# Performance work log

Hardware: AMD Instinct MI355X
Metric: run time of the kernel (lower is better)

## Reference

```python
import jax, jax.numpy as jnp
import numpy as np

D = 128        # d_model (LayerNorm(128) hardcoded)
N_HEADS = 4
DIM_K = D // N_HEADS           # 32
HD = DIM_K // N_HEADS          # 8 = per-group dim after reshape(-1, B, S, HD)
NORM_FACT = 1.0 / np.sqrt(DIM_K)
HIDDEN = 512
LN_EPS = 1e-5
NEG_INF = -1e30


def layer_norm(x, g, b):
    mu = jnp.mean(x, axis=-1, keepdims=True)
    var = jnp.mean((x - mu) ** 2, axis=-1, keepdims=True)
    return (x - mu) * jax.lax.rsqrt(var + LN_EPS) * g + b


def lower_median(x):
    # torch.median(dim=-1) returns the LOWER of the two middle values for even n
    n = x.shape[-1]
    return jnp.sort(x, axis=-1)[..., (n - 1) // 2][..., None]


def cross_cov_attention(x, y, Wq, bq, Wk, bk, Wv, bv, Wo, bo):
    # x: query-side input [B,S,D]; y: key/value-side input [B,S,D]
    B, S, _ = x.shape
    Q = (x @ Wq + bq).reshape(-1, B, S, HD)   # [16,B,S,8] (raw row-major reshape, as in torch)
    K = (y @ Wk + bk).reshape(-1, B, S, HD)
    V = (y @ Wv + bv).reshape(-1, B, S, HD)
    Qn = Q / jnp.maximum(jnp.linalg.norm(Q, axis=-1, keepdims=True), 1e-12)
    Kn = K / jnp.maximum(jnp.linalg.norm(K, axis=-1, keepdims=True), 1e-12)
    # channel-wise cross-covariance: Q^T K over tokens -> [16,B,8,8]
    scores = jnp.einsum('gbsd,gbse->gbde', Qn, Kn) * NORM_FACT
    # median-threshold mask: keep entries strictly above the (lower) median of each row
    med = lower_median(scores)
    scores = jnp.where(scores - med > 0, scores, NEG_INF)
    probs = jax.nn.softmax(scores, axis=-1)
    # probs @ V^T -> [16,B,8,S]
    ao = jnp.einsum('gbde,gbse->gbds', probs, V)
    # torch: .transpose(-2,-1).transpose(1,2).view(B,S,-1)  == axes (g,b,d,s)->(g,s,b,d)->reshape
    ao = ao.transpose(0, 3, 1, 2).reshape(B, S, -1)  # [B,S,128]
    return ao @ Wo + bo


def setup_inputs() -> dict:
    key = jax.random.key(0)
    ks = jax.random.split(key, 16)
    B, S = 32, 4096
    s = 1.0 / np.sqrt(D)
    inp = {
        'q': jax.random.normal(ks[0], (B, S, D), jnp.float32),
        'v': jax.random.normal(ks[1], (B, S, D), jnp.float32),
        'Wq': jax.random.normal(ks[2], (D, D), jnp.float32) * s,
        'bq': jnp.zeros((D,), jnp.float32),
        'Wk': jax.random.normal(ks[3], (D, D), jnp.float32) * s,
        'bk': jnp.zeros((D,), jnp.float32),
        'Wv': jax.random.normal(ks[4], (D, D), jnp.float32) * s,
        'bv': jnp.zeros((D,), jnp.float32),
        'Wo': jax.random.normal(ks[5], (D, D), jnp.float32) * s,
        'bo': jnp.zeros((D,), jnp.float32),
        'ln_g': jnp.ones((D,), jnp.float32),
        'ln_b': jnp.zeros((D,), jnp.float32),
        'W1': jax.random.normal(ks[6], (D, HIDDEN), jnp.float32) * s,
        'b1': jnp.zeros((HIDDEN,), jnp.float32),
        'W2': jax.random.normal(ks[7], (HIDDEN, D), jnp.float32) * (1.0 / np.sqrt(HIDDEN)),
        'b2': jnp.zeros((D,), jnp.float32),
    }
    return inp


def reference(q, v, Wq, bq, Wk, bk, Wv, bv, Wo, bo, ln_g, ln_b, W1, b1, W2, b2):
    # Decoder.forward: add_norm(v, attn, y=q) -> add_norm(ffn) -> + v
    attn = cross_cov_attention(v, q, Wq, bq, Wk, bk, Wv, bv, Wo, bo)
    h = layer_norm(v + attn, ln_g, ln_b)          # dropout = identity (eval)
    ffn = jax.nn.gelu(h @ W1 + b1, approximate=False) @ W2 + b2
    h2 = layer_norm(h + ffn, ln_g, ln_b)          # same Add_Norm (shared LayerNorm params)
    return h2 + v
```

## Files before the change

### kernel.cpp

```cpp
#include <hip/hip_runtime.h>
#include <math.h>


typedef __bf16 bf16x8 __attribute__((ext_vector_type(8)));
typedef float f32x4 __attribute__((ext_vector_type(4)));
typedef unsigned short u16x8 __attribute__((ext_vector_type(8)));
typedef unsigned int u32x2 __attribute__((ext_vector_type(2)));
typedef unsigned int u32x4 __attribute__((ext_vector_type(4)));
typedef unsigned short ushort_t;

static constexpr int  DM   = 128;
static constexpr long NTOK = 131072;
static constexpr float NORMF = 0.17677669529663687f;

__device__ __forceinline__ unsigned short f2b(float x) {
    __bf16 b = (__bf16)x;
    return __builtin_bit_cast(unsigned short, b);
}
__device__ __forceinline__ float b2f(unsigned short h) {
    return __builtin_bit_cast(float, ((unsigned)h) << 16);
}
__device__ __forceinline__ float b2f_lo(unsigned u) {
    return __builtin_bit_cast(float, u << 16);
}
__device__ __forceinline__ float b2f_hi(unsigned u) {
    return __builtin_bit_cast(float, u & 0xffff0000u);
}
__device__ __forceinline__ unsigned pack2(float a, float b) {
    return (unsigned)f2b(a) | ((unsigned)f2b(b) << 16);
}
__device__ __forceinline__ f32x4 mfma16(bf16x8 a, bf16x8 b, f32x4 c) {
    return __builtin_amdgcn_mfma_f32_16x16x32_bf16(a, b, c, 0, 0, 0);
}
__device__ __forceinline__ int xb_off(int tok, int chunk) {
    int c = (chunk & 8) | ((chunk ^ tok) & 7);
    return tok * 128 + c * 8;
}
__device__ __forceinline__ float gelu_f(float x) {
    float x2 = x * x;
    float y = -x * fmaf(0.0713548162f, x2, 1.5957691216f);
    float e = __expf(y);
    return x * __builtin_amdgcn_rcpf(1.0f + e);
}

__global__ __launch_bounds__(256)
void k_wcvt(const float* __restrict__ W1, const float* __restrict__ W2,
            const float* __restrict__ Wo, const float* __restrict__ Wq,
            const float* __restrict__ Wk, const float* __restrict__ Wv,
            ushort_t* __restrict__ W1t, ushort_t* __restrict__ W2t,
            ushort_t* __restrict__ Wot,
            ushort_t* __restrict__ Wqh, ushort_t* __restrict__ Wql,
            ushort_t* __restrict__ Wkh, ushort_t* __restrict__ Wkl,
            ushort_t* __restrict__ Wvh, ushort_t* __restrict__ Wvl)
{
    int frag = blockIdx.x * 4 + (threadIdx.x >> 6);
    int l = threadIdx.x & 63;
    int lr = l & 15, lg = l >> 4;
    u16x8 v;
    if (frag < 128) {
        int ht = frag >> 2, ks = frag & 3;
        #pragma unroll
        for (int j = 0; j < 8; ++j)
            v[j] = f2b(W1[(ks * 32 + lg * 8 + j) * 512 + ht * 16 + lr]);
        *(u16x8*)(W1t + ((long)frag * 64 + l) * 8) = v;
    } else if (frag < 256) {
        int f = frag - 128;
        int ot = f >> 4, ks = f & 15;
        #pragma unroll
        for (int j = 0; j < 8; ++j)
            v[j] = f2b(W2[(ks * 32 + lg * 8 + j) * 128 + ot * 16 + lr]);
        *(u16x8*)(W2t + ((long)f * 64 + l) * 8) = v;
    } else if (frag < 288) {
        int f = frag - 256;
        int ot = f >> 2, ks = f & 3;
        #pragma unroll
        for (int j = 0; j < 8; ++j)
            v[j] = f2b(Wo[(ks * 32 + lg * 8 + j) * 128 + ot * 16 + lr]);
        *(u16x8*)(Wot + ((long)f * 64 + l) * 8) = v;
    } else {
        int f = frag - 288;
        const float* S = (f < 32) ? Wq : (f < 64) ? Wk : Wv;
        ushort_t* dh = (f < 32) ? Wqh : (f < 64) ? Wkh : Wvh;
        ushort_t* dl = (f < 32) ? Wql : (f < 64) ? Wkl : Wvl;
        int fl = f & 31, ot = fl >> 2, ks = fl & 3;
        u16x8 vh, vl;
        #pragma unroll
        for (int j = 0; j < 8; ++j) {
            float x = S[(ks * 32 + lg * 8 + j) * 128 + ot * 16 + lr];
            __bf16 bh = (__bf16)x;
            vh[j] = __builtin_bit_cast(unsigned short, bh);
            vl[j] = f2b(x - (float)bh);
        }
        *(u16x8*)(dh + ((long)fl * 64 + l) * 8) = vh;
        *(u16x8*)(dl + ((long)fl * 64 + l) * 8) = vl;
    }
}

__global__ __launch_bounds__(256, 2)
void k_qkvs(const float* __restrict__ qin, const float* __restrict__ vin,
            const ushort_t* __restrict__ Wqh, const ushort_t* __restrict__ Wql,
            const ushort_t* __restrict__ Wkh, const ushort_t* __restrict__ Wkl,
            const ushort_t* __restrict__ Wvh, const ushort_t* __restrict__ Wvl,
            const float* __restrict__ bq, const float* __restrict__ bk,
            const float* __restrict__ bv,
            ushort_t* __restrict__ Vbf, float* __restrict__ scoreacc)
{
    __shared__ __align__(16) char smem[65536];
    ushort_t* vhi = (ushort_t*)smem;
    ushort_t* vlo = vhi + 8192;
    ushort_t* qhi = vlo + 8192;
    ushort_t* qlo = qhi + 8192;
    ushort_t* Vt  = (ushort_t*)smem;
    float*    red = (float*)(smem + 16384);

    const int tid = threadIdx.x;
    const int w = tid >> 6, l = tid & 63;
    const int lr = l & 15, lg = l >> 4;
    const long tok0 = (long)blockIdx.x * 64;

    #pragma unroll
    for (int i = 0; i < 4; ++i) {
        int e = tid + i * 256;
        int tok = e >> 4, c = e & 15;
        long base = (tok0 + tok) * DM + c * 8;
        int xo = xb_off(tok, c);
        {
            float4 a0 = *(const float4*)(vin + base);
            float4 a1 = *(const float4*)(vin + base + 4);
            float xs[8] = {a0.x, a0.y, a0.z, a0.w, a1.x, a1.y, a1.z, a1.w};
            u16x8 hi, lo;
            #pragma unroll
            for (int jj = 0; jj < 8; ++jj) {
                __bf16 bh = (__bf16)xs[jj];
                hi[jj] = __builtin_bit_cast(unsigned short, bh);
                lo[jj] = f2b(xs[jj] - (float)bh);
            }
            *(u16x8*)(vhi + xo) = hi;
            *(u16x8*)(vlo + xo) = lo;
        }
        {
            float4 a0 = *(const float4*)(qin + base);
            float4 a1 = *(const float4*)(qin + base + 4);
            float xs[8] = {a0.x, a0.y, a0.z, a0.w, a1.x, a1.y, a1.z, a1.w};
            u16x8 hi, lo;
            #pragma unroll
            for (int jj = 0; jj < 8; ++jj) {
                __bf16 bh = (__bf16)xs[jj];
                hi[jj] = __builtin_bit_cast(unsigned short, bh);
                lo[jj] = f2b(xs[jj] - (float)bh);
            }
            *(u16x8*)(qhi + xo) = hi;
            *(u16x8*)(qlo + xo) = lo;
        }
    }
    __syncthreads();

    float qv[2][4][4];
    {
        f32x4 acc[2][4];
        #pragma unroll
        for (int ot = 0; ot < 2; ++ot)
            #pragma unroll
            for (int tt = 0; tt < 4; ++tt) acc[ot][tt] = (f32x4){0,0,0,0};
        #pragma unroll
        for (int ks = 0; ks < 4; ++ks) {
            bf16x8 wh[2], wl[2];
            #pragma unroll
            for (int ot = 0; ot < 2; ++ot) {
                int fi = (((w * 2 + ot) * 4 + ks) * 64 + l) * 8;
                wh[ot] = *(const bf16x8*)(Wqh + fi);
                wl[ot] = *(const bf16x8*)(Wql + fi);
            }
            #pragma unroll
            for (int tt = 0; tt < 4; ++tt) {
                int xo = xb_off(tt * 16 + lr, ks * 4 + lg);
                bf16x8 xh = *(const bf16x8*)(vhi + xo);
                bf16x8 xl = *(const bf16x8*)(vlo + xo);
                #pragma unroll
                for (int ot = 0; ot < 2; ++ot) {
                    acc[ot][tt] = mfma16(wh[ot], xh, acc[ot][tt]);
                    acc[ot][tt] = mfma16(wh[ot], xl, acc[ot][tt]);
                    acc[ot][tt] = mfma16(wl[ot], xh, acc[ot][tt]);
                }
            }
        }
        #pragma unroll
        for (int ot = 0; ot < 2; ++ot) {
            f32x4 bqv = *(const f32x4*)(bq + w * 32 + ot * 16 + lg * 4);
            #pragma unroll
            for (int tt = 0; tt < 4; ++tt) {
                float s2 = 0.f;
                #pragma unroll
                for (int r = 0; r < 4; ++r) {
                    float x = acc[ot][tt][r] + bqv[r];
                    qv[ot][tt][r] = x;
                    s2 = fmaf(x, x, s2);
                }
                s2 += __shfl_xor(s2, 16);
                float inv = 1.0f / fmaxf(sqrtf(s2), 1e-12f);
                #pragma unroll
                for (int r = 0; r < 4; ++r) qv[ot][tt][r] *= inv;
            }
        }
    }

    float vv[2][4][4];
    float part[4][8];
    #pragma unroll
    for (int r = 0; r < 4; ++r)
        #pragma unroll
        for (int e = 0; e < 8; ++e) part[r][e] = 0.f;
    {
        f32x4 acck[2][4], accv[2][4];
        #pragma unroll
        for (int ot = 0; ot < 2; ++ot)
            #pragma unroll
            for (int tt = 0; tt < 4; ++tt) {
                acck[ot][tt] = (f32x4){0,0,0,0};
                accv[ot][tt] = (f32x4){0,0,0,0};
            }
        #pragma unroll
        for (int ks = 0; ks < 4; ++ks) {
            bf16x8 whk[2], wlk[2], whv[2];
            #pragma unroll
            for (int ot = 0; ot < 2; ++ot) {
                int fi = (((w * 2 + ot) * 4 + ks) * 64 + l) * 8;
                whk[ot] = *(const bf16x8*)(Wkh + fi);
                wlk[ot] = *(const bf16x8*)(Wkl + fi);
                whv[ot] = *(const bf16x8*)(Wvh + fi);
            }
            #pragma unroll
            for (int tt = 0; tt < 4; ++tt) {
                int xo = xb_off(tt * 16 + lr, ks * 4 + lg);
                bf16x8 xh = *(const bf16x8*)(qhi + xo);
                bf16x8 xl = *(const bf16x8*)(qlo + xo);
                #pragma unroll
                for (int ot = 0; ot < 2; ++ot) {
                    acck[ot][tt] = mfma16(whk[ot], xh, acck[ot][tt]);
                    acck[ot][tt] = mfma16(whk[ot], xl, acck[ot][tt]);
                    acck[ot][tt] = mfma16(wlk[ot], xh, acck[ot][tt]);
                    accv[ot][tt] = mfma16(whv[ot], xh, accv[ot][tt]);
                    accv[ot][tt] = mfma16(whv[ot], xl, accv[ot][tt]);
                }
            }
        }
        const int h0 = (lg & 1) * 4;
        #pragma unroll
        for (int ot = 0; ot < 2; ++ot) {
            f32x4 bkv = *(const f32x4*)(bk + w * 32 + ot * 16 + lg * 4);
            f32x4 bvv = *(const f32x4*)(bv + w * 32 + ot * 16 + lg * 4);
            #pragma unroll
            for (int tt = 0; tt < 4; ++tt) {
                float kq[4];
                float s2 = 0.f;
                #pragma unroll
                for (int r = 0; r < 4; ++r) {
                    float x = acck[ot][tt][r] + bkv[r];
                    kq[r] = x;
                    s2 = fmaf(x, x, s2);
                    vv[ot][tt][r] = accv[ot][tt][r] + bvv[r];
                }
                s2 += __shfl_xor(s2, 16);
                float inv = 1.0f / fmaxf(sqrtf(s2), 1e-12f);
                #pragma unroll
                for (int r = 0; r < 4; ++r) kq[r] *= inv;
                float ko[4];
                #pragma unroll
                for (int r = 0; r < 4; ++r) ko[r] = __shfl_xor(kq[r], 16);
                float ke[8];
                #pragma unroll
                for (int r = 0; r < 4; ++r) {
                    ke[h0 + r] = kq[r];
                    ke[(h0 ^ 4) + r] = ko[r];
                }
                #pragma unroll
                for (int r = 0; r < 4; ++r)
                    #pragma unroll
                    for (int e = 0; e < 8; ++e)
                        part[r][e] = fmaf(qv[ot][tt][r], ke[e], part[r][e]);
            }
        }
    }
    #pragma unroll
    for (int r = 0; r < 4; ++r)
        #pragma unroll
        for (int e = 0; e < 8; ++e) {
            float p = part[r][e];
            p += __shfl_xor(p, 1);
            p += __shfl_xor(p, 2);
            p += __shfl_xor(p, 4);
            p += __shfl_xor(p, 8);
            part[r][e] = p;
        }
    __syncthreads();

    #pragma unroll
    for (int ot = 0; ot < 2; ++ot) {
        int oc0 = w * 32 + ot * 16 + lg * 4;
        int ch = oc0 >> 3;
        #pragma unroll
        for (int tt = 0; tt < 4; ++tt) {
            int tok = tt * 16 + lr;
            int cz = (ch & 8) | ((ch ^ tok) & 7);
            u32x2 pk = {pack2(vv[ot][tt][0], vv[ot][tt][1]),
                        pack2(vv[ot][tt][2], vv[ot][tt][3])};
            *(u32x2*)(Vt + tok * 128 + cz * 8 + (oc0 & 7)) = pk;
        }
    }
    if (lr == 0) {
        #pragma unroll
        for (int r = 0; r < 4; ++r)
            #pragma unroll
            for (int e = 0; e < 8; ++e)
                red[(w * 4 + lg) * 33 + r * 8 + e] = part[r][e];
    }
    __syncthreads();

    #pragma unroll
    for (int i = 0; i < 4; ++i) {
        int e = tid + i * 256;
        int tok = e >> 4, c = e & 15;
        int cz = (c & 8) | ((c ^ tok) & 7);
        u16x8 val = *(const u16x8*)(Vt + tok * 128 + cz * 8);
        *(u16x8*)(Vbf + (tok0 + tok) * DM + c * 8) = val;
    }
    if (tid < 64) {
        int d = tid >> 3, e = tid & 7;
        int par = d >> 2, r = d & 3;
        float s = 0.f;
        #pragma unroll
        for (int ww = 0; ww < 4; ++ww)
            s += red[(ww * 4 + par) * 33 + r * 8 + e] +
                 red[(ww * 4 + par + 2) * 33 + r * 8 + e];
        scoreacc[(long)blockIdx.x * 64 + tid] = s;
    }
}

__global__ __launch_bounds__(64)
void k_medsoft(const float* __restrict__ scoreacc, ushort_t* __restrict__ probsb)
{
    __shared__ float sc[64], pl[64];
    const int p = blockIdx.x, tid = threadIdx.x;
    const float* s0 = scoreacc + (long)p * 256;
    sc[tid] = (s0[tid] + s0[64 + tid] + s0[128 + tid] + s0[192 + tid]) * NORMF;
    __syncthreads();
    if (tid < 8) {
        float row[8], st[8];
        #pragma unroll
        for (int e = 0; e < 8; ++e) { row[e] = sc[tid * 8 + e]; st[e] = row[e]; }
        for (int a = 1; a < 8; ++a) {
            float v = st[a]; int b = a - 1;
            while (b >= 0 && st[b] > v) { st[b + 1] = st[b]; --b; }
            st[b + 1] = v;
        }
        float med = st[3];
        float mv[8]; float mx = -3.0e38f;
        #pragma unroll
        for (int e = 0; e < 8; ++e) {
            mv[e] = (row[e] - med > 0.f) ? row[e] : -1e30f;
            mx = fmaxf(mx, mv[e]);
        }
        float z = 0.f, ex[8];
        #pragma unroll
        for (int e = 0; e < 8; ++e) { ex[e] = expf(mv[e] - mx); z += ex[e]; }
        float iz = 1.f / z;
        #pragma unroll
        for (int e = 0; e < 8; ++e) pl[tid * 8 + e] = ex[e] * iz;
    }
    __syncthreads();
    probsb[(long)p * 64 + tid] = f2b(pl[tid]);
}

__global__ __launch_bounds__(256, 4)
void k_tail(const ushort_t* __restrict__ Vbf, const ushort_t* __restrict__ Pb,
            const ushort_t* __restrict__ Wot, const float* __restrict__ bo,
            const ushort_t* __restrict__ W1t, const float* __restrict__ b1,
            const ushort_t* __restrict__ W2t, const float* __restrict__ b2,
            const float* __restrict__ lng, const float* __restrict__ lnb,
            const float* __restrict__ vres, float* __restrict__ out)
{
    __shared__ __align__(16) char smem[37376];
    ushort_t* Xb  = (ushort_t*)smem;
    ushort_t* Vg  = (ushort_t*)(smem + 16384);
    ushort_t* Hp  = (ushort_t*)(smem + 16384);
    ushort_t* Hid = (ushort_t*)(smem + 16384);
    ushort_t* Plb = (ushort_t*)(smem + 32768);
    float* pS  = (float*)(smem + 32768);
    float* pQ  = pS + 256;
    float* muS = pQ + 256;
    float* rsS = muS + 64;

    const int tid = threadIdx.x;
    const int w = tid >> 6, l = tid & 63;
    const int lr = l & 15, lg = l >> 4;
    const int wid = ((blockIdx.x & 7) << 8) | (blockIdx.x >> 3);
    const long T0 = (long)wid * 64;
    const int g  = (int)(T0 >> 13);
    const int r0 = (int)((T0 & 8191) >> 5);

    {
        int e = tid * 8;
        u16x8 pv = *(const u16x8*)(Pb + (long)g * 2048 + e);
        *(u16x8*)(Plb + (e >> 6) * 72 + (e & 63)) = pv;
    }
    #pragma unroll
    for (int i = 0; i < 4; ++i) {
        int e = tid + i * 256;
        int ri = e >> 4, c = e & 15;
        int hb = ri >> 5, bm = (ri >> 1) & 15, rr = ri & 1;
        long t = ((long)(g * 32 + hb * 16 + bm)) * 256 + r0 + rr;
        u16x8 val = *(const u16x8*)(Vbf + t * DM + c * 8);
        int cz = (c & 8) | ((c ^ (ri >> 1)) & 7);
        *(u16x8*)(Vg + ri * 128 + cz * 8) = val;
    }
    __syncthreads();

    #pragma unroll
    for (int i = 0; i < 4; ++i) {
        int e = tid + i * 256;
        int ti = e >> 4, bm = e & 15;
        int jj = (ti & 31) >> 1, hb = ti & 1, rr = ti >> 5;
        int ri = hb * 32 + bm * 2 + rr;
        int cz = (jj & 8) | ((jj ^ (ri >> 1)) & 7);
        u16x8 v8 = *(const u16x8*)(Vg + ri * 128 + cz * 8);
        float vf[8];
        #pragma unroll
        for (int e2 = 0; e2 < 8; ++e2) vf[e2] = b2f(v8[e2]);
        const ushort_t* pp = Plb + (hb * 16 + bm) * 72;
        float sd[8];
        #pragma unroll
        for (int d = 0; d < 8; ++d) {
            u16x8 pr = *(const u16x8*)(pp + d * 8);
            float s = 0.f;
            #pragma unroll
            for (int e2 = 0; e2 < 8; ++e2) s = fmaf(b2f(pr[e2]), vf[e2], s);
            sd[d] = s;
        }
        u32x4 po = {pack2(sd[0], sd[1]), pack2(sd[2], sd[3]),
                    pack2(sd[4], sd[5]), pack2(sd[6], sd[7])};
        *(u32x4*)(Xb + xb_off(ti, bm)) = po;
    }
    __syncthreads();

    float sums[4] = {0, 0, 0, 0}, sqs[4] = {0, 0, 0, 0};
    #pragma unroll
    for (int ot = 0; ot < 2; ++ot) {
        bf16x8 aw[4];
        #pragma unroll
        for (int ks = 0; ks < 4; ++ks)
            aw[ks] = *(const bf16x8*)(Wot +
                ((long)((w * 2 + ot) * 4 + ks) * 64 + l) * 8);
        const int oc0 = w * 32 + ot * 16 + lg * 4;
        f32x4 bov = *(const f32x4*)(bo + oc0);
        #pragma unroll
        for (int tt = 0; tt < 4; ++tt) {
            f32x4 acc = (f32x4){0, 0, 0, 0};
            int tok = tt * 16 + lr;
            #pragma unroll
            for (int ks = 0; ks < 4; ++ks) {
                bf16x8 bfrag = *(const bf16x8*)(Xb + xb_off(tok, ks * 4 + lg));
                acc = mfma16(aw[ks], bfrag, acc);
            }
            long gtok = T0 + tok;
            f32x4 xv = *(const f32x4*)(vres + gtok * DM + oc0);
            float hp[4];
            #pragma unroll
            for (int r = 0; r < 4; ++r) {
                hp[r] = acc[r] + bov[r] + xv[r];
                sums[tt] += hp[r];
                sqs[tt] = fmaf(hp[r], hp[r], sqs[tt]);
            }
            int ch = oc0 >> 3;
            int cz = (ch & 8) | ((ch ^ tok) & 7);
            u32x2 pk = {pack2(hp[0], hp[1]), pack2(hp[2], hp[3])};
            *(u32x2*)(Hp + tok * 128 + cz * 8 + (oc0 & 7)) = pk;
        }
    }
    #pragma unroll
    for (int tt = 0; tt < 4; ++tt) {
        sums[tt] += __shfl_xor(sums[tt], 16);
        sums[tt] += __shfl_xor(sums[tt], 32);
        sqs[tt]  += __shfl_xor(sqs[tt], 16);
        sqs[tt]  += __shfl_xor(sqs[tt], 32);
    }
    #pragma unroll
    for (int tt = 0; tt < 4; ++tt)
        if (lg == tt) { pS[(w * 4 + tt) * 16 + lr] = sums[tt];
                        pQ[(w * 4 + tt) * 16 + lr] = sqs[tt]; }
    __syncthreads();
    if (tid < 64) {
        float s = pS[tid] + pS[64 + tid] + pS[128 + tid] + pS[192 + tid];
        float q = pQ[tid] + pQ[64 + tid] + pQ[128 + tid] + pQ[192 + tid];
        float mu = s * 0.0078125f;
        float var = q * 0.0078125f - mu * mu;
        muS[tid] = mu;
        rsS[tid] = rsqrtf(var + 1e-5f);
    }
    __syncthreads();

    #pragma unroll
    for (int tt = 0; tt < 4; ++tt) {
        int tok = tt * 16 + lr;
        float mu = muS[tok], rs = rsS[tok];
        #pragma unroll
        for (int ot = 0; ot < 2; ++ot) {
            int oc0 = w * 32 + ot * 16 + lg * 4;
            f32x4 g4 = *(const f32x4*)(lng + oc0);
            f32x4 bb4 = *(const f32x4*)(lnb + oc0);
            int ch = oc0 >> 3;
            int cz = (ch & 8) | ((ch ^ tok) & 7);
            int off = tok * 128 + cz * 8 + (oc0 & 7);
            u32x2 hpv = *(const u32x2*)(Hp + off);
            float hr[4] = {b2f_lo(hpv[0]), b2f_hi(hpv[0]),
                           b2f_lo(hpv[1]), b2f_hi(hpv[1])};
            float hf[4];
            #pragma unroll
            for (int r = 0; r < 4; ++r)
                hf[r] = (hr[r] - mu) * rs * g4[r] + bb4[r];
            u32x2 pk = {pack2(hf[0], hf[1]), pack2(hf[2], hf[3])};
            *(u32x2*)(Xb + off) = pk;
        }
    }
    __syncthreads();

    f32x4 oacc[4][2];
    #pragma unroll
    for (int tt = 0; tt < 4; ++tt) {
        oacc[tt][0] = (f32x4){0,0,0,0};
        oacc[tt][1] = (f32x4){0,0,0,0};
    }
    for (int sl = 0; sl < 4; ++sl) {
        #pragma unroll
        for (int hh = 0; hh < 2; ++hh) {
            bf16x8 a1[4];
            #pragma unroll
            for (int ks = 0; ks < 4; ++ks)
                a1[ks] = *(const bf16x8*)(W1t +
                    ((long)((sl * 8 + w * 2 + hh) * 4 + ks) * 64 + l) * 8);
            f32x4 b1v = *(const f32x4*)(b1 + (sl * 8 + w * 2 + hh) * 16 + lg * 4);
            #pragma unroll
            for (int tt = 0; tt < 4; ++tt) {
                f32x4 acc = (f32x4){0, 0, 0, 0};
                int tok = tt * 16 + lr;
                #pragma unroll
                for (int ks = 0; ks < 4; ++ks) {
                    bf16x8 bfrag = *(const bf16x8*)(Xb + xb_off(tok, ks * 4 + lg));
                    acc = mfma16(a1[ks], bfrag, acc);
                }
                float gg[4];
                #pragma unroll
                for (int r = 0; r < 4; ++r)
                    gg[r] = gelu_f(acc[r] + b1v[r]);
                int hc0 = w * 32 + hh * 16 + lg * 4;
                int ch = hc0 >> 3;
                int cz = (ch & 8) | ((ch ^ tok) & 7);
                u32x2 pk = {pack2(gg[0], gg[1]), pack2(gg[2], gg[3])};
                *(u32x2*)(Hid + tok * 128 + cz * 8 + (hc0 & 7)) = pk;
            }
        }
        __syncthreads();
        #pragma unroll
        for (int op = 0; op < 2; ++op) {
            bf16x8 a2[4];
            #pragma unroll
            for (int kl = 0; kl < 4; ++kl)
                a2[kl] = *(const bf16x8*)(W2t +
                    ((long)((w * 2 + op) * 16 + sl * 4 + kl) * 64 + l) * 8);
            #pragma unroll
            for (int tt = 0; tt < 4; ++tt) {
                int tok = tt * 16 + lr;
                #pragma unroll
                for (int kl = 0; kl < 4; ++kl) {
                    bf16x8 bfrag = *(const bf16x8*)(Hid + xb_off(tok, kl * 4 + lg));
                    oacc[tt][op] = mfma16(a2[kl], bfrag, oacc[tt][op]);
                }
            }
        }
        __syncthreads();
    }

    #pragma unroll
    for (int tt = 0; tt < 4; ++tt) {
        int tok = tt * 16 + lr;
        float s = 0.f, q = 0.f;
        #pragma unroll
        for (int ot = 0; ot < 2; ++ot) {
            int oc0 = w * 32 + ot * 16 + lg * 4;
            f32x4 b2v = *(const f32x4*)(b2 + oc0);
            int ch = oc0 >> 3;
            int cz = (ch & 8) | ((ch ^ tok) & 7);
            u32x2 hpv = *(const u32x2*)(Xb + tok * 128 + cz * 8 + (oc0 & 7));
            float hr[4] = {b2f_lo(hpv[0]), b2f_hi(hpv[0]),
                           b2f_lo(hpv[1]), b2f_hi(hpv[1])};
            #pragma unroll
            for (int r = 0; r < 4; ++r) {
                float vvv = oacc[tt][ot][r] + b2v[r] + hr[r];
                s += vvv; q = fmaf(vvv, vvv, q);
            }
        }
        sums[tt] = s; sqs[tt] = q;
    }
    #pragma unroll
    for (int tt = 0; tt < 4; ++tt) {
        sums[tt] += __shfl_xor(sums[tt], 16);
        sums[tt] += __shfl_xor(sums[tt], 32);
        sqs[tt]  += __shfl_xor(sqs[tt], 16);
        sqs[tt]  += __shfl_xor(sqs[tt], 32);
    }
    #pragma unroll
    for (int tt = 0; tt < 4; ++tt)
        if (lg == tt) { pS[(w * 4 + tt) * 16 + lr] = sums[tt];
                        pQ[(w * 4 + tt) * 16 + lr] = sqs[tt]; }
    __syncthreads();
    if (tid < 64) {
        float s = pS[tid] + pS[64 + tid] + pS[128 + tid] + pS[192 + tid];
        float q = pQ[tid] + pQ[64 + tid] + pQ[128 + tid] + pQ[192 + tid];
        float mu = s * 0.0078125f;
        float var = q * 0.0078125f - mu * mu;
        muS[tid] = mu;
        rsS[tid] = rsqrtf(var + 1e-5f);
    }
    __syncthreads();
    #pragma unroll
    for (int tt = 0; tt < 4; ++tt) {
        int tok = tt * 16 + lr;
        long gtok = T0 + tok;
        float mu = muS[tok], rs = rsS[tok];
        #pragma unroll
        for (int ot = 0; ot < 2; ++ot) {
            int oc0 = w * 32 + ot * 16 + lg * 4;
            f32x4 b2v = *(const f32x4*)(b2 + oc0);
            f32x4 g4 = *(const f32x4*)(lng + oc0);
            f32x4 bb4 = *(const f32x4*)(lnb + oc0);
            int ch = oc0 >> 3;
            int cz = (ch & 8) | ((ch ^ tok) & 7);
            u32x2 hpv = *(const u32x2*)(Xb + tok * 128 + cz * 8 + (oc0 & 7));
            float hr[4] = {b2f_lo(hpv[0]), b2f_hi(hpv[0]),
                           b2f_lo(hpv[1]), b2f_hi(hpv[1])};
            f32x4 vv4 = *(const f32x4*)(vres + gtok * DM + oc0);
            f32x4 o;
            #pragma unroll
            for (int r = 0; r < 4; ++r) {
                float vvv = oacc[tt][ot][r] + b2v[r] + hr[r];
                o[r] = (vvv - mu) * rs * g4[r] + bb4[r] + vv4[r];
            }
            *(f32x4*)(out + gtok * DM + oc0) = o;
        }
    }
}

extern "C" void kernel_launch(void* const* d_in, const int* in_sizes, int n_in,
                              void* d_out, int out_size, void* d_ws, size_t ws_size,
                              hipStream_t stream)
{
    const float* q   = (const float*)d_in[0];
    const float* v   = (const float*)d_in[1];
    const float* Wq  = (const float*)d_in[2];
    const float* bq  = (const float*)d_in[3];
    const float* Wk  = (const float*)d_in[4];
    const float* bk  = (const float*)d_in[5];
    const float* Wv  = (const float*)d_in[6];
    const float* bv  = (const float*)d_in[7];
    const float* Wo  = (const float*)d_in[8];
    const float* bo  = (const float*)d_in[9];
    const float* lng = (const float*)d_in[10];
    const float* lnb = (const float*)d_in[11];
    const float* W1  = (const float*)d_in[12];
    const float* b1  = (const float*)d_in[13];
    const float* W2  = (const float*)d_in[14];
    const float* b2  = (const float*)d_in[15];
    float* out = (float*)d_out;

    char* W = (char*)d_ws;
    ushort_t* Vbf      = (ushort_t*)(W);
    float*    scoreacc = (float*)(W + 33554432);
    ushort_t* probsb   = (ushort_t*)(W + 34078720);
    char* wbase = W + 34209792;
    ushort_t* Wqh = (ushort_t*)(wbase);
    ushort_t* Wql = (ushort_t*)(wbase + 32768);
    ushort_t* Wkh = (ushort_t*)(wbase + 65536);
    ushort_t* Wkl = (ushort_t*)(wbase + 98304);
    ushort_t* Wvh = (ushort_t*)(wbase + 131072);
    ushort_t* Wvl = (ushort_t*)(wbase + 163840);
    ushort_t* W1t = (ushort_t*)(wbase + 196608);
    ushort_t* W2t = (ushort_t*)(wbase + 327680);
    ushort_t* Wot = (ushort_t*)(wbase + 458752);

    dim3 blk(256);
    k_wcvt<<<96, blk, 0, stream>>>(W1, W2, Wo, Wq, Wk, Wv,
                                   W1t, W2t, Wot, Wqh, Wql, Wkh, Wkl, Wvh, Wvl);
    k_qkvs<<<2048, blk, 0, stream>>>(q, v, Wqh, Wql, Wkh, Wkl, Wvh, Wvl,
                                     bq, bk, bv, Vbf, scoreacc);
    k_medsoft<<<512, dim3(64), 0, stream>>>(scoreacc, probsb);
    k_tail<<<2048, blk, 0, stream>>>(Vbf, probsb, Wot, bo, W1t, b1, W2t, b2,
                                     lng, lnb, v, out);
}
```

Baseline: 182.4 us.

## Fold first LayerNorm into W1 GEMM epilogue and drop V low-part MFMA

Folds the first LayerNorm's gamma into the bf16 W1 fragments and precomputes per-hidden sums G1 and C1, so the FFN1 GEMM runs on the raw residual Hp. Normalization becomes a per-token affine applied in the epilogue, which removes a full LDS normalize-and-rewrite pass and one barrier in the tail kernel. Separately, the V projection drops its bf16 low-part correction MFMA, trading accuracy for fewer MFMAs. This adds a tiny extra launch, recomputes h in the final LN passes, and risks cancellation error from applying mean subtraction after the GEMM in bf16.

```diff
diff --git a/kernel.cpp b/kernel.cpp
--- a/kernel.cpp
+++ b/kernel.cpp
@@ -47,6 +47,7 @@
 void k_wcvt(const float* __restrict__ W1, const float* __restrict__ W2,
             const float* __restrict__ Wo, const float* __restrict__ Wq,
             const float* __restrict__ Wk, const float* __restrict__ Wv,
+            const float* __restrict__ lng,
             ushort_t* __restrict__ W1t, ushort_t* __restrict__ W2t,
             ushort_t* __restrict__ Wot,
             ushort_t* __restrict__ Wqh, ushort_t* __restrict__ Wql,
@@ -60,8 +61,10 @@
     if (frag < 128) {
         int ht = frag >> 2, ks = frag & 3;
         #pragma unroll
-        for (int j = 0; j < 8; ++j)
-            v[j] = f2b(W1[(ks * 32 + lg * 8 + j) * 512 + ht * 16 + lr]);
+        for (int j = 0; j < 8; ++j) {
+            int k = ks * 32 + lg * 8 + j;
+            v[j] = f2b(lng[k] * W1[(long)k * 512 + ht * 16 + lr]);
+        }
         *(u16x8*)(W1t + ((long)frag * 64 + l) * 8) = v;
     } else if (frag < 256) {
         int f = frag - 128;
@@ -96,11 +99,27 @@
     }
 }
 
+__global__ __launch_bounds__(256)
+void k_lnfold(const float* __restrict__ W1, const float* __restrict__ lng,
+              const float* __restrict__ lnb, const float* __restrict__ b1,
+              float* __restrict__ G1, float* __restrict__ C1)
+{
+    int j = blockIdx.x * 256 + threadIdx.x;
+    float gs = 0.f, bs = 0.f;
+    for (int k = 0; k < 128; ++k) {
+        float wv = W1[(long)k * 512 + j];
+        gs = fmaf(lng[k], wv, gs);
+        bs = fmaf(lnb[k], wv, bs);
+    }
+    G1[j] = gs;
+    C1[j] = bs + b1[j];
+}
+
 __global__ __launch_bounds__(256, 2)
 void k_qkvs(const float* __restrict__ qin, const float* __restrict__ vin,
             const ushort_t* __restrict__ Wqh, const ushort_t* __restrict__ Wql,
             const ushort_t* __restrict__ Wkh, const ushort_t* __restrict__ Wkl,
-            const ushort_t* __restrict__ Wvh, const ushort_t* __restrict__ Wvl,
+            const ushort_t* __restrict__ Wvh,
             const float* __restrict__ bq, const float* __restrict__ bk,
             const float* __restrict__ bv,
             ushort_t* __restrict__ Vbf, float* __restrict__ scoreacc)
@@ -240,7 +259,6 @@
                     acck[ot][tt] = mfma16(whk[ot], xl, acck[ot][tt]);
                     acck[ot][tt] = mfma16(wlk[ot], xh, acck[ot][tt]);
                     accv[ot][tt] = mfma16(whv[ot], xh, accv[ot][tt]);
-                    accv[ot][tt] = mfma16(whv[ot], xl, accv[ot][tt]);
                 }
             }
         }
@@ -374,7 +392,8 @@
 __global__ __launch_bounds__(256, 4)
 void k_tail(const ushort_t* __restrict__ Vbf, const ushort_t* __restrict__ Pb,
             const ushort_t* __restrict__ Wot, const float* __restrict__ bo,
-            const ushort_t* __restrict__ W1t, const float* __restrict__ b1,
+            const ushort_t* __restrict__ W1t, const float* __restrict__ G1,
+            const float* __restrict__ C1,
             const ushort_t* __restrict__ W2t, const float* __restrict__ b2,
             const float* __restrict__ lng, const float* __restrict__ lnb,
             const float* __restrict__ vres, float* __restrict__ out)
@@ -383,12 +402,13 @@
     ushort_t* Xb  = (ushort_t*)smem;
     ushort_t* Vg  = (ushort_t*)(smem + 16384);
     ushort_t* Hp  = (ushort_t*)(smem + 16384);
-    ushort_t* Hid = (ushort_t*)(smem + 16384);
     ushort_t* Plb = (ushort_t*)(smem + 32768);
-    float* pS  = (float*)(smem + 32768);
-    float* pQ  = pS + 256;
-    float* muS = pQ + 256;
-    float* rsS = muS + 64;
+    float* pS   = (float*)(smem + 32768);
+    float* pQ   = pS + 256;
+    float* mu1S = pQ + 256;
+    float* rs1S = mu1S + 64;
+    float* mu2S = rs1S + 64;
+    float* rs2S = mu2S + 64;
 
     const int tid = threadIdx.x;
     const int w = tid >> 6, l = tid & 63;
@@ -493,33 +513,8 @@
         float q = pQ[tid] + pQ[64 + tid] + pQ[128 + tid] + pQ[192 + tid];
         float mu = s * 0.0078125f;
         float var = q * 0.0078125f - mu * mu;
-        muS[tid] = mu;
-        rsS[tid] = rsqrtf(var + 1e-5f);
-    }
-    __syncthreads();
-
-    #pragma unroll
-    for (int tt = 0; tt < 4; ++tt) {
-        int tok = tt * 16 + lr;
-        float mu = muS[tok], rs = rsS[tok];
-        #pragma unroll
-        for (int ot = 0; ot < 2; ++ot) {
-            int oc0 = w * 32 + ot * 16 + lg * 4;
-            f32x4 g4 = *(const f32x4*)(lng + oc0);
-            f32x4 bb4 = *(const f32x4*)(lnb + oc0);
-            int ch = oc0 >> 3;
-            int cz = (ch & 8) | ((ch ^ tok) & 7);
-            int off = tok * 128 + cz * 8 + (oc0 & 7);
-            u32x2 hpv = *(const u32x2*)(Hp + off);
-            float hr[4] = {b2f_lo(hpv[0]), b2f_hi(hpv[0]),
-                           b2f_lo(hpv[1]), b2f_hi(hpv[1])};
-            float hf[4];
-            #pragma unroll
-            for (int r = 0; r < 4; ++r)
-                hf[r] = (hr[r] - mu) * rs * g4[r] + bb4[r];
-            u32x2 pk = {pack2(hf[0], hf[1]), pack2(hf[2], hf[3])};
-            *(u32x2*)(Xb + off) = pk;
-        }
+        mu1S[tid] = mu;
+        rs1S[tid] = rsqrtf(var + 1e-5f);
     }
     __syncthreads();
 
@@ -537,25 +532,31 @@
             for (int ks = 0; ks < 4; ++ks)
                 a1[ks] = *(const bf16x8*)(W1t +
                     ((long)((sl * 8 + w * 2 + hh) * 4 + ks) * 64 + l) * 8);
-            f32x4 b1v = *(const f32x4*)(b1 + (sl * 8 + w * 2 + hh) * 16 + lg * 4);
+            int hcb = (sl * 8 + w * 2 + hh) * 16 + lg * 4;
+            f32x4 G1v = *(const f32x4*)(G1 + hcb);
+            f32x4 C1v = *(const f32x4*)(C1 + hcb);
             #pragma unroll
             for (int tt = 0; tt < 4; ++tt) {
                 f32x4 acc = (f32x4){0, 0, 0, 0};
                 int tok = tt * 16 + lr;
                 #pragma unroll
                 for (int ks = 0; ks < 4; ++ks) {
-                    bf16x8 bfrag = *(const bf16x8*)(Xb + xb_off(tok, ks * 4 + lg));
+                    bf16x8 bfrag = *(const bf16x8*)(Hp + xb_off(tok, ks * 4 + lg));
                     acc = mfma16(a1[ks], bfrag, acc);
                 }
+                float mu1 = mu1S[tok], rs1 = rs1S[tok];
+                float mneg = -mu1 * rs1;
                 float gg[4];
                 #pragma unroll
-                for (int r = 0; r < 4; ++r)
-                    gg[r] = gelu_f(acc[r] + b1v[r]);
+                for (int r = 0; r < 4; ++r) {
+                    float pre = fmaf(rs1, acc[r], fmaf(mneg, G1v[r], C1v[r]));
+                    gg[r] = gelu_f(pre);
+                }
                 int hc0 = w * 32 + hh * 16 + lg * 4;
                 int ch = hc0 >> 3;
                 int cz = (ch & 8) | ((ch ^ tok) & 7);
                 u32x2 pk = {pack2(gg[0], gg[1]), pack2(gg[2], gg[3])};
-                *(u32x2*)(Hid + tok * 128 + cz * 8 + (hc0 & 7)) = pk;
+                *(u32x2*)(Xb + tok * 128 + cz * 8 + (hc0 & 7)) = pk;
             }
         }
         __syncthreads();
@@ -571,7 +572,7 @@
                 int tok = tt * 16 + lr;
                 #pragma unroll
                 for (int kl = 0; kl < 4; ++kl) {
-                    bf16x8 bfrag = *(const bf16x8*)(Hid + xb_off(tok, kl * 4 + lg));
+                    bf16x8 bfrag = *(const bf16x8*)(Xb + xb_off(tok, kl * 4 + lg));
                     oacc[tt][op] = mfma16(a2[kl], bfrag, oacc[tt][op]);
                 }
             }
@@ -582,50 +583,8 @@
     #pragma unroll
     for (int tt = 0; tt < 4; ++tt) {
         int tok = tt * 16 + lr;
+        float mu1 = mu1S[tok], rs1 = rs1S[tok];
         float s = 0.f, q = 0.f;
-        #pragma unroll
-        for (int ot = 0; ot < 2; ++ot) {
-            int oc0 = w * 32 + ot * 16 + lg * 4;
-            f32x4 b2v = *(const f32x4*)(b2 + oc0);
-            int ch = oc0 >> 3;
-            int cz = (ch & 8) | ((ch ^ tok) & 7);
-            u32x2 hpv = *(const u32x2*)(Xb + tok * 128 + cz * 8 + (oc0 & 7));
-            float hr[4] = {b2f_lo(hpv[0]), b2f_hi(hpv[0]),
-                           b2f_lo(hpv[1]), b2f_hi(hpv[1])};
-            #pragma unroll
-            for (int r = 0; r < 4; ++r) {
-                float vvv = oacc[tt][ot][r] + b2v[r] + hr[r];
-                s += vvv; q = fmaf(vvv, vvv, q);
-            }
-        }
-        sums[tt] = s; sqs[tt] = q;
-    }
-    #pragma unroll
-    for (int tt = 0; tt < 4; ++tt) {
-        sums[tt] += __shfl_xor(sums[tt], 16);
-        sums[tt] += __shfl_xor(sums[tt], 32);
-        sqs[tt]  += __shfl_xor(sqs[tt], 16);
-        sqs[tt]  += __shfl_xor(sqs[tt], 32);
-    }
-    #pragma unroll
-    for (int tt = 0; tt < 4; ++tt)
-        if (lg == tt) { pS[(w * 4 + tt) * 16 + lr] = sums[tt];
-                        pQ[(w * 4 + tt) * 16 + lr] = sqs[tt]; }
-    __syncthreads();
-    if (tid < 64) {
-        float s = pS[tid] + pS[64 + tid] + pS[128 + tid] + pS[192 + tid];
-        float q = pQ[tid] + pQ[64 + tid] + pQ[128 + tid] + pQ[192 + tid];
-        float mu = s * 0.0078125f;
-        float var = q * 0.0078125f - mu * mu;
-        muS[tid] = mu;
-        rsS[tid] = rsqrtf(var + 1e-5f);
-    }
-    __syncthreads();
-    #pragma unroll
-    for (int tt = 0; tt < 4; ++tt) {
-        int tok = tt * 16 + lr;
-        long gtok = T0 + tok;
-        float mu = muS[tok], rs = rsS[tok];
         #pragma unroll
         for (int ot = 0; ot < 2; ++ot) {
             int oc0 = w * 32 + ot * 16 + lg * 4;
@@ -634,15 +593,63 @@
             f32x4 bb4 = *(const f32x4*)(lnb + oc0);
             int ch = oc0 >> 3;
             int cz = (ch & 8) | ((ch ^ tok) & 7);
-            u32x2 hpv = *(const u32x2*)(Xb + tok * 128 + cz * 8 + (oc0 & 7));
+            u32x2 hpv = *(const u32x2*)(Hp + tok * 128 + cz * 8 + (oc0 & 7));
+            float hr[4] = {b2f_lo(hpv[0]), b2f_hi(hpv[0]),
+                           b2f_lo(hpv[1]), b2f_hi(hpv[1])};
+            #pragma unroll
+            for (int r = 0; r < 4; ++r) {
+                float h = (hr[r] - mu1) * rs1 * g4[r] + bb4[r];
+                float vvv = oacc[tt][ot][r] + b2v[r] + h;
+                s += vvv; q = fmaf(vvv, vvv, q);
+            }
+        }
+        sums[tt] = s; sqs[tt] = q;
+    }
+    #pragma unroll
+    for (int tt = 0; tt < 4; ++tt) {
+        sums[tt] += __shfl_xor(sums[tt], 16);
+        sums[tt] += __shfl_xor(sums[tt], 32);
+        sqs[tt]  += __shfl_xor(sqs[tt], 16);
+        sqs[tt]  += __shfl_xor(sqs[tt], 32);
+    }
+    #pragma unroll
+    for (int tt = 0; tt < 4; ++tt)
+        if (lg == tt) { pS[(w * 4 + tt) * 16 + lr] = sums[tt];
+                        pQ[(w * 4 + tt) * 16 + lr] = sqs[tt]; }
+    __syncthreads();
+    if (tid < 64) {
+        float s = pS[tid] + pS[64 + tid] + pS[128 + tid] + pS[192 + tid];
+        float q = pQ[tid] + pQ[64 + tid] + pQ[128 + tid] + pQ[192 + tid];
+        float mu = s * 0.0078125f;
+        float var = q * 0.0078125f - mu * mu;
+        mu2S[tid] = mu;
+        rs2S[tid] = rsqrtf(var + 1e-5f);
+    }
+    __syncthreads();
+    #pragma unroll
+    for (int tt = 0; tt < 4; ++tt) {
+        int tok = tt * 16 + lr;
+        long gtok = T0 + tok;
+        float mu1 = mu1S[tok], rs1 = rs1S[tok];
+        float mu2 = mu2S[tok], rs2 = rs2S[tok];
+        #pragma unroll
+        for (int ot = 0; ot < 2; ++ot) {
+            int oc0 = w * 32 + ot * 16 + lg * 4;
+            f32x4 b2v = *(const f32x4*)(b2 + oc0);
+            f32x4 g4 = *(const f32x4*)(lng + oc0);
+            f32x4 bb4 = *(const f32x4*)(lnb + oc0);
+            int ch = oc0 >> 3;
+            int cz = (ch & 8) | ((ch ^ tok) & 7);
+            u32x2 hpv = *(const u32x2*)(Hp + tok * 128 + cz * 8 + (oc0 & 7));
             float hr[4] = {b2f_lo(hpv[0]), b2f_hi(hpv[0]),
                            b2f_lo(hpv[1]), b2f_hi(hpv[1])};
             f32x4 vv4 = *(const f32x4*)(vres + gtok * DM + oc0);
             f32x4 o;
             #pragma unroll
             for (int r = 0; r < 4; ++r) {
-                float vvv = oacc[tt][ot][r] + b2v[r] + hr[r];
-                o[r] = (vvv - mu) * rs * g4[r] + bb4[r] + vv4[r];
+                float h = (hr[r] - mu1) * rs1 * g4[r] + bb4[r];
+                float vvv = oacc[tt][ot][r] + b2v[r] + h;
+                o[r] = (vvv - mu2) * rs2 * g4[r] + bb4[r] + vv4[r];
             }
             *(f32x4*)(out + gtok * DM + oc0) = o;
         }
@@ -685,13 +692,16 @@
     ushort_t* W1t = (ushort_t*)(wbase + 196608);
     ushort_t* W2t = (ushort_t*)(wbase + 327680);
     ushort_t* Wot = (ushort_t*)(wbase + 458752);
+    float*    G1  = (float*)(wbase + 491520);
+    float*    C1  = (float*)(wbase + 493568);
 
     dim3 blk(256);
-    k_wcvt<<<96, blk, 0, stream>>>(W1, W2, Wo, Wq, Wk, Wv,
+    k_wcvt<<<96, blk, 0, stream>>>(W1, W2, Wo, Wq, Wk, Wv, lng,
                                    W1t, W2t, Wot, Wqh, Wql, Wkh, Wkl, Wvh, Wvl);
-    k_qkvs<<<2048, blk, 0, stream>>>(q, v, Wqh, Wql, Wkh, Wkl, Wvh, Wvl,
+    k_lnfold<<<2, blk, 0, stream>>>(W1, lng, lnb, b1, G1, C1);
+    k_qkvs<<<2048, blk, 0, stream>>>(q, v, Wqh, Wql, Wkh, Wkl, Wvh,
                                      bq, bk, bv, Vbf, scoreacc);
     k_medsoft<<<512, dim3(64), 0, stream>>>(scoreacc, probsb);
-    k_tail<<<2048, blk, 0, stream>>>(Vbf, probsb, Wot, bo, W1t, b1, W2t, b2,
-                                     lng, lnb, v, out);
-}
+    k_tail<<<2048, blk, 0, stream>>>(Vbf, probsb, Wot, bo, W1t, G1, C1,
+                                     W2t, b2, lng, lnb, v, out);
+}
```

After: 189.9 us. 1.04x slower.
